# Kernel optimization log

Hardware: AMD Instinct MI355X
Metric: run time of the kernel (lower is better)

The kernel has to match this reference:

```python
import jax, jax.numpy as jnp
import numpy as np

B, L, D, H, E, K = 4, 2048, 1024, 2048, 8, 2


def _mlp(x, w1, b1, w2, b2):
    # Mlp: Linear -> GELU(tanh) -> Linear (dropout disabled / eval mode)
    h = jax.nn.gelu(x @ w1 + b1, approximate=True)
    return h @ w2 + b2


def setup_inputs() -> dict:
    key = jax.random.key(0)
    ks = jax.random.split(key, 16)
    s = 0.02
    inp = {
        "x": jax.random.normal(ks[0], (B, L, D), dtype=jnp.float32),
        "task_ids": jax.random.randint(ks[1], (B,), 0, 9),
        # gate: Linear(D,H) -> GELU -> Linear(H,E)  (zero-init in source; randomized here for a meaningful routing test)
        "gw1": jax.random.normal(ks[2], (D, H), dtype=jnp.float32) * s,
        "gb1": jnp.zeros((H,), dtype=jnp.float32),
        "gw2": jax.random.normal(ks[3], (H, E), dtype=jnp.float32) * s,
        "gb2": jnp.zeros((E,), dtype=jnp.float32),
        # routed experts, stacked [E, ...]
        "We1": jax.random.normal(ks[4], (E, D, H), dtype=jnp.float32) * s,
        "be1": jnp.zeros((E, H), dtype=jnp.float32),
        "We2": jax.random.normal(ks[5], (E, H, D), dtype=jnp.float32) * s,
        "be2": jnp.zeros((E, D), dtype=jnp.float32),
        # shared expert
        "Ws1": jax.random.normal(ks[6], (D, H), dtype=jnp.float32) * s,
        "bs1": jnp.zeros((H,), dtype=jnp.float32),
        "Ws2": jax.random.normal(ks[7], (H, D), dtype=jnp.float32) * s,
        "bs2": jnp.zeros((D,), dtype=jnp.float32),
    }
    return inp


def reference(x, task_ids, gw1, gb1, gw2, gb2, We1, be1, We2, be2, Ws1, bs1, Ws2, bs2):
    bsz, length, d = x.shape
    T = bsz * length
    xf = x.reshape(T, d)

    # ---- top-k gating (single gate: moe_multiple_gate=False) ----
    logits = jax.nn.gelu(xf @ gw1 + gb1, approximate=False) @ gw2 + gb2  # [T, E]
    scores = jax.nn.softmax(logits, axis=-1)
    topk_w, topk_idx = jax.lax.top_k(scores, K)  # [T, K]
    # dense gate matrix: scatter top-k weights back (matches compute_gating's gates)
    rows = jnp.arange(T)[:, None]
    gates = jnp.zeros_like(scores).at[rows, topk_idx].set(topk_w)  # [T, E]

    # ---- shared expert (always applied) ----
    out = _mlp(xf, Ws1, bs1, Ws2, bs2)

    # ---- routed experts: dense-equivalent of sort/dispatch/scatter-combine ----
    # y += sum_e gates[:, e] * expert_e(x); loop over small fixed E to bound memory
    for e in range(E):
        out = out + gates[:, e:e + 1] * _mlp(xf, We1[e], be1[e], We2[e], be2[e])

    return out.reshape(bsz, length, d)
```

## Files before the change

kernel.cpp:

```cpp
#include <hip/hip_runtime.h>
#include <hip/hip_bf16.h>


using bf16 = __hip_bfloat16;
typedef __attribute__((ext_vector_type(8))) short short8;
typedef __attribute__((ext_vector_type(4))) float float4v;

#define T_TOK 8192
#define DDIM  1024
#define HDIM  2048
#define NEXP  8

__device__ __forceinline__ float bf2f(short s) {
  unsigned u = ((unsigned)(unsigned short)s) << 16;
  return __builtin_bit_cast(float, u);
}
__device__ __forceinline__ unsigned short f2bf(float f) {
  unsigned u = __builtin_bit_cast(unsigned, f);
  unsigned r = (u + 0x7fffu + ((u >> 16) & 1u)) >> 16;
  return (unsigned short)r;
}
__device__ __forceinline__ float gelu_erf_f(float x) {
  return 0.5f * x * (1.0f + erff(x * 0.70710678118654752f));
}
__device__ __forceinline__ float gelu_tanh_f(float x) {
  float t = tanhf(0.7978845608028654f * (x + 0.044715f * x * x * x));
  return 0.5f * x * (1.0f + t);
}
__device__ __forceinline__ void gld_lds16(const bf16* g, bf16* l) {
  __builtin_amdgcn_global_load_lds(
      (const __attribute__((address_space(1))) void*)g,
      (__attribute__((address_space(3))) void*)l, 16, 0, 0);
}

__global__ __launch_bounds__(256) void cast_split_x(
    const float* __restrict__ x, bf16* __restrict__ xh, bf16* __restrict__ xl)
{
  long i = ((long)blockIdx.x * 256 + threadIdx.x) * 4;
  float4v v = *(const float4v*)(x + i);
  short4 h, l;
  short* hp = (short*)&h; short* lp = (short*)&l;
  #pragma unroll
  for (int j = 0; j < 4; ++j) {
    unsigned short hb = f2bf(v[j]);
    hp[j] = (short)hb;
    lp[j] = (short)f2bf(v[j] - bf2f((short)hb));
  }
  *(short4*)((short*)xh + i) = h;
  *(short4*)((short*)xl + i) = l;
}

template<bool SPLIT>
__global__ __launch_bounds__(256) void transpose_cast(
    const float* __restrict__ in, bf16* __restrict__ out,
    bf16* __restrict__ outl, int R, int C)
{
  __shared__ float tile[32][33];
  long b = blockIdx.z;
  const float* ip = in + b * (long)R * C;
  short* op = (short*)out + b * (long)R * C;
  short* opl = SPLIT ? (short*)outl + b * (long)R * C : nullptr;
  int c0 = blockIdx.x * 32, r0 = blockIdx.y * 32;
  int tx = threadIdx.x & 31, ty = threadIdx.x >> 5;
  #pragma unroll
  for (int i = ty; i < 32; i += 8)
    tile[i][tx] = ip[(long)(r0 + i) * C + c0 + tx];
  __syncthreads();
  #pragma unroll
  for (int i = ty; i < 32; i += 8) {
    float v = tile[tx][i];
    unsigned short hb = f2bf(v);
    op[(long)(c0 + i) * R + r0 + tx] = (short)hb;
    if (SPLIT)
      opl[(long)(c0 + i) * R + r0 + tx] = (short)f2bf(v - bf2f((short)hb));
  }
}

template<int ACT, typename OutT, int GATHER, bool WEIGHTED, bool SPLIT>
__global__ __launch_bounds__(256) void gemm_bt(
    const bf16* __restrict__ A, const bf16* __restrict__ Bt,
    const bf16* __restrict__ Al, const bf16* __restrict__ Btl,
    const float* __restrict__ bias, OutT* __restrict__ Cmat,
    int M, int N, int Kd, int ldA,
    long strideB, long strideBias,
    const int* __restrict__ perm, const int* __restrict__ counts,
    const float* __restrict__ wslot)
{
  __shared__ __align__(16) bf16 lA[128 * 32];
  __shared__ __align__(16) bf16 lB[128 * 32];
  __shared__ int permT[128];

  const int tid = threadIdx.x;
  const int tile_n = blockIdx.x, tile_m = blockIdx.y, z = blockIdx.z;

  int Meff = M;
  if (GATHER) {
    const int* perm_z = perm + (long)z * T_TOK;
    Meff = counts[z];
    if (tile_m * 128 >= Meff) return;
    if (tid < 128) {
      int i = tile_m * 128 + tid;
      permT[tid] = perm_z[i < Meff ? i : (Meff - 1)];
    }
    __syncthreads();
  }
  const float* biasz = bias + (long)z * strideBias;

  const int i0 = tid >> 2;
  const int kc = (tid & 3) * 8;
  long rowA0, rowA1;
  if (GATHER) {
    int p0 = permT[i0], p1 = permT[i0 + 64];
    rowA0 = (GATHER == 1) ? (p0 >> 1) : p0;
    rowA1 = (GATHER == 1) ? (p1 >> 1) : p1;
  } else {
    rowA0 = (long)tile_m * 128 + i0;
    rowA1 = rowA0 + 64;
  }
  bf16* lA0 = &lA[tid * 8];
  bf16* lA1 = &lA[(tid + 256) * 8];
  bf16* lB0 = &lB[tid * 8];
  bf16* lB1 = &lB[(tid + 256) * 8];

  const int lane = tid & 63;
  const int wave = tid >> 6;
  const int wm = (wave & 1) * 64;
  const int wn = (wave >> 1) * 64;
  const int fr = lane & 15;
  const int fk = (lane >> 4) * 8;

  float4v acc[4][4];
  #pragma unroll
  for (int i = 0; i < 4; ++i)
    #pragma unroll
    for (int j = 0; j < 4; ++j) acc[i][j] = {0.f, 0.f, 0.f, 0.f};

  #pragma unroll 1
  for (int ps = 0; ps < (SPLIT ? 3 : 1); ++ps) {
    const bf16* Ap = (SPLIT && ps == 2) ? Al : A;
    const bf16* Bp = (SPLIT && ps == 1) ? Btl : Bt;
    const bf16* aBase0 = Ap + rowA0 * ldA + kc;
    const bf16* aBase1 = Ap + rowA1 * ldA + kc;
    const bf16* bBase0 = Bp + (long)z * strideB
                       + ((long)tile_n * 128 + i0) * Kd + kc;
    const bf16* bBase1 = bBase0 + (long)64 * Kd;

    for (int k0 = 0; k0 < Kd; k0 += 32) {
      gld_lds16(aBase0 + k0, lA0);
      gld_lds16(aBase1 + k0, lA1);
      gld_lds16(bBase0 + k0, lB0);
      gld_lds16(bBase1 + k0, lB1);
      __syncthreads();

      short8 af[4], bfr[4];
      #pragma unroll
      for (int mi = 0; mi < 4; ++mi)
        af[mi] = *(const short8*)&lA[(wm + mi * 16 + fr) * 32 + fk];
      #pragma unroll
      for (int ni = 0; ni < 4; ++ni)
        bfr[ni] = *(const short8*)&lB[(wn + ni * 16 + fr) * 32 + fk];
      #pragma unroll
      for (int mi = 0; mi < 4; ++mi)
        #pragma unroll
        for (int ni = 0; ni < 4; ++ni)
          acc[mi][ni] = __builtin_amdgcn_mfma_f32_16x16x32_bf16(
              af[mi], bfr[ni], acc[mi][ni], 0, 0, 0);
      __syncthreads();
    }
  }

  const int rq = (lane >> 4) * 4;
  #pragma unroll
  for (int mi = 0; mi < 4; ++mi) {
    #pragma unroll
    for (int r = 0; r < 4; ++r) {
      int irow = wm + mi * 16 + rq + r;
      int gi = tile_m * 128 + irow;
      long crow;
      bool valid = true;
      float w = 1.f;
      if (GATHER) {
        valid = gi < Meff;
        int p = permT[irow];
        crow = p;
        if (WEIGHTED) w = valid ? wslot[p] : 0.f;
      } else {
        crow = gi;
      }
      if (valid) {
        #pragma unroll
        for (int ni = 0; ni < 4; ++ni) {
          int gcol = tile_n * 128 + wn + ni * 16 + fr;
          float v = acc[mi][ni][r] + biasz[gcol];
          if (ACT == 1) v = gelu_erf_f(v);
          else if (ACT == 2) v = gelu_tanh_f(v);
          if (WEIGHTED) v *= w;
          long cidx = crow * (long)N + gcol;
          if (sizeof(OutT) == 4) ((float*)Cmat)[cidx] = v;
          else ((unsigned short*)Cmat)[cidx] = f2bf(v);
        }
      }
    }
  }
}

__global__ __launch_bounds__(256) void logits_kernel(
    const float* __restrict__ G1, const float* __restrict__ gw2,
    const float* __restrict__ gb2, int* __restrict__ tidx,
    float* __restrict__ wslot)
{
  int wv = threadIdx.x >> 6, lane = threadIdx.x & 63;
  int t = blockIdx.x * 4 + wv;
  const float* grow = G1 + (long)t * HDIM;
  float acc[NEXP];
  #pragma unroll
  for (int e = 0; e < NEXP; ++e) acc[e] = 0.f;
  for (int j = 0; j < HDIM / 64; ++j) {
    int h = j * 64 + lane;
    float g = grow[h];
    float4v w0 = *(const float4v*)&gw2[h * NEXP];
    float4v w1 = *(const float4v*)&gw2[h * NEXP + 4];
    #pragma unroll
    for (int e = 0; e < 4; ++e) {
      acc[e]     += g * w0[e];
      acc[e + 4] += g * w1[e];
    }
  }
  #pragma unroll
  for (int off = 32; off >= 1; off >>= 1)
    #pragma unroll
    for (int e = 0; e < NEXP; ++e) acc[e] += __shfl_xor(acc[e], off);

  if (lane == 0) {
    float lg[NEXP];
    #pragma unroll
    for (int e = 0; e < NEXP; ++e) lg[e] = acc[e] + gb2[e];
    int i1 = 0;
    for (int e = 1; e < NEXP; ++e) if (lg[e] > lg[i1]) i1 = e;
    int i2 = (i1 == 0) ? 1 : 0;
    for (int e = 0; e < NEXP; ++e) {
      if (e == i1) continue;
      if (lg[e] > lg[i2]) i2 = e;
    }
    float m = lg[i1], s = 0.f;
    #pragma unroll
    for (int e = 0; e < NEXP; ++e) s += expf(lg[e] - m);
    float inv = 1.f / s;
    tidx[2 * t]     = i1;
    tidx[2 * t + 1] = i2;
    wslot[2 * t]     = expf(lg[i1] - m) * inv;
    wslot[2 * t + 1] = expf(lg[i2] - m) * inv;
  }
}

__global__ __launch_bounds__(256) void dispatch_kernel(
    const int* __restrict__ tidx, int* __restrict__ counts,
    int* __restrict__ perm)
{
  int t = blockIdx.x * 256 + threadIdx.x;
  int lane = threadIdx.x & 63;
  #pragma unroll
  for (int k = 0; k < 2; ++k) {
    int e = tidx[2 * t + k];
    #pragma unroll
    for (int ex = 0; ex < NEXP; ++ex) {
      unsigned long long m = __ballot(e == ex);
      if (m) {
        int leader = __ffsll((unsigned long long)m) - 1;
        int base = 0;
        if (lane == leader) base = atomicAdd(&counts[ex], __popcll(m));
        base = __shfl(base, leader);
        if (e == ex) {
          int pos = base + __popcll(m & ((1ULL << lane) - 1ULL));
          perm[ex * T_TOK + pos] = 2 * t + k;
        }
      }
    }
  }
}

__global__ __launch_bounds__(256) void combine_kernel(
    const bf16* __restrict__ Rout, float* __restrict__ out)
{
  long idx = (long)blockIdx.x * 256 + threadIdx.x;
  long t = idx >> 7;
  long dc = idx & 127;
  const short* rs = (const short*)Rout;
  short8 a = *(const short8*)&rs[(2 * t) * DDIM + dc * 8];
  short8 b = *(const short8*)&rs[(2 * t + 1) * DDIM + dc * 8];
  float* op = out + idx * 8;
  float4v o0 = *(const float4v*)op;
  float4v o1 = *(const float4v*)(op + 4);
  #pragma unroll
  for (int j = 0; j < 4; ++j) o0[j] += bf2f(a[j]) + bf2f(b[j]);
  #pragma unroll
  for (int j = 0; j < 4; ++j) o1[j] += bf2f(a[j + 4]) + bf2f(b[j + 4]);
  *(float4v*)op = o0;
  *(float4v*)(op + 4) = o1;
}

extern "C" void kernel_launch(void* const* d_in, const int* in_sizes, int n_in,
                              void* d_out, int out_size, void* d_ws, size_t ws_size,
                              hipStream_t stream)
{
  const float* x   = (const float*)d_in[0];
  const float* gw1 = (const float*)d_in[2];
  const float* gb1 = (const float*)d_in[3];
  const float* gw2 = (const float*)d_in[4];
  const float* gb2 = (const float*)d_in[5];
  const float* We1 = (const float*)d_in[6];
  const float* be1 = (const float*)d_in[7];
  const float* We2 = (const float*)d_in[8];
  const float* be2 = (const float*)d_in[9];
  const float* Ws1 = (const float*)d_in[10];
  const float* bs1 = (const float*)d_in[11];
  const float* Ws2 = (const float*)d_in[12];
  const float* bs2 = (const float*)d_in[13];
  float* out = (float*)d_out;

  char* ws = (char*)d_ws;
  bf16*  xb     = (bf16*)(ws + 0);
  bf16*  We1t   = (bf16*)(ws + 16777216);
  bf16*  Rout   = (bf16*)(ws + 16777216);
  bf16*  We2t   = (bf16*)(ws + 50331648);
  bf16*  Ws1t   = (bf16*)(ws + 83886080);
  bf16*  Ws2t   = (bf16*)(ws + 88080384);
  int*   counts = (int*)(ws + 92274688);
  float* wslot  = (float*)(ws + 92275712);
  int*   perm   = (int*)(ws + 92341248);
  bf16*  xl     = (bf16*)(ws + 92603392);
  bf16*  gw1h   = (bf16*)(ws + 109380608);
  bf16*  gw1l   = (bf16*)(ws + 113574912);
  int*   tidx   = (int*)(ws + 113574912);
  float* G1     = (float*)(ws + 117769216);
  bf16*  S1     = (bf16*)(ws + 117769216);
  bf16*  Hrt    = (bf16*)(ws + 117769216);

  hipMemsetAsync(counts, 0, NEXP * sizeof(int), stream);

  dim3 blk(256);
  cast_split_x<<<dim3((T_TOK * DDIM) / 1024), blk, 0, stream>>>(x, xb, xl);
  transpose_cast<true ><<<dim3(HDIM/32, DDIM/32, 1), blk, 0, stream>>>(gw1, gw1h, gw1l, DDIM, HDIM);
  transpose_cast<false><<<dim3(HDIM/32, DDIM/32, 1), blk, 0, stream>>>(Ws1, Ws1t, nullptr, DDIM, HDIM);
  transpose_cast<false><<<dim3(DDIM/32, HDIM/32, 1), blk, 0, stream>>>(Ws2, Ws2t, nullptr, HDIM, DDIM);
  transpose_cast<false><<<dim3(HDIM/32, DDIM/32, NEXP), blk, 0, stream>>>(We1, We1t, nullptr, DDIM, HDIM);
  transpose_cast<false><<<dim3(DDIM/32, HDIM/32, NEXP), blk, 0, stream>>>(We2, We2t, nullptr, HDIM, DDIM);

  gemm_bt<1, float, 0, false, true><<<dim3(HDIM/128, T_TOK/128, 1), blk, 0, stream>>>(
      xb, gw1h, xl, gw1l, gb1, G1, T_TOK, HDIM, DDIM, DDIM, 0, 0,
      nullptr, nullptr, nullptr);
  logits_kernel<<<dim3(T_TOK / 4), blk, 0, stream>>>(G1, gw2, gb2, tidx, wslot);
  dispatch_kernel<<<dim3(T_TOK / 256), blk, 0, stream>>>(tidx, counts, perm);
  gemm_bt<2, bf16, 0, false, false><<<dim3(HDIM/128, T_TOK/128, 1), blk, 0, stream>>>(
      xb, Ws1t, nullptr, nullptr, bs1, S1, T_TOK, HDIM, DDIM, DDIM, 0, 0,
      nullptr, nullptr, nullptr);
  gemm_bt<0, float, 0, false, false><<<dim3(DDIM/128, T_TOK/128, 1), blk, 0, stream>>>(
      S1, Ws2t, nullptr, nullptr, bs2, out, T_TOK, DDIM, HDIM, HDIM, 0, 0,
      nullptr, nullptr, nullptr);
  gemm_bt<2, bf16, 1, false, false><<<dim3(HDIM/128, T_TOK/128, NEXP), blk, 0, stream>>>(
      xb, We1t, nullptr, nullptr, be1, Hrt, T_TOK, HDIM, DDIM, DDIM,
      (long)HDIM * DDIM, HDIM, perm, counts, nullptr);
  gemm_bt<0, bf16, 2, true, false><<<dim3(DDIM/128, T_TOK/128, NEXP), blk, 0, stream>>>(
      Hrt, We2t, nullptr, nullptr, be2, Rout, T_TOK, DDIM, HDIM, HDIM,
      (long)DDIM * HDIM, DDIM, perm, counts, wslot);
  combine_kernel<<<dim3((T_TOK * DDIM) / 2048), blk, 0, stream>>>(Rout, out);
}
```

Measured before the change: 901.6 us.

## Fuse routed-expert combine into shared-expert GEMM epilogue and XOR-swizzle LDS tiles

The routed-expert GEMMs now run before the shared-expert MLP. The final shared GEMM epilogue reads the two weighted bf16 routed outputs per token and adds them before writing fp32 output, so the separate combine kernel and its extra read-modify-write pass over the output go away. The LDS tile layout also gets an XOR swizzle of the 16-byte k-chunk by row index, on both the global-to-LDS writes and the MFMA fragment reads, to cut bank conflicts on the 64-byte row stride. The trade-off is that the fused epilogue does scalar, less-coalesced bf16 loads of Rout inside the GEMM, and the new launch order depends on Rout staying intact while later kernels write their buffers.

```diff
diff --git a/kernel.cpp b/kernel.cpp
--- a/kernel.cpp
+++ b/kernel.cpp
@@ -76,7 +76,7 @@
   }
 }
 
-template<int ACT, typename OutT, int GATHER, bool WEIGHTED, bool SPLIT>
+template<int ACT, typename OutT, int GATHER, bool WEIGHTED, bool SPLIT, bool COMBINE>
 __global__ __launch_bounds__(256) void gemm_bt(
     const bf16* __restrict__ A, const bf16* __restrict__ Bt,
     const bf16* __restrict__ Al, const bf16* __restrict__ Btl,
@@ -84,7 +84,7 @@
     int M, int N, int Kd, int ldA,
     long strideB, long strideBias,
     const int* __restrict__ perm, const int* __restrict__ counts,
-    const float* __restrict__ wslot)
+    const float* __restrict__ wslot, const bf16* __restrict__ RoutC)
 {
   __shared__ __align__(16) bf16 lA[128 * 32];
   __shared__ __align__(16) bf16 lB[128 * 32];
@@ -107,7 +107,7 @@
   const float* biasz = bias + (long)z * strideBias;
 
   const int i0 = tid >> 2;
-  const int kc = (tid & 3) * 8;
+  const int kc = (((tid & 3) ^ ((tid >> 2) & 3))) * 8;
   long rowA0, rowA1;
   if (GATHER) {
     int p0 = permT[i0], p1 = permT[i0 + 64];
@@ -127,7 +127,7 @@
   const int wm = (wave & 1) * 64;
   const int wn = (wave >> 1) * 64;
   const int fr = lane & 15;
-  const int fk = (lane >> 4) * 8;
+  const int sw = (((lane >> 4) ^ (lane & 3))) * 8;
 
   float4v acc[4][4];
   #pragma unroll
@@ -155,10 +155,10 @@
       short8 af[4], bfr[4];
       #pragma unroll
       for (int mi = 0; mi < 4; ++mi)
-        af[mi] = *(const short8*)&lA[(wm + mi * 16 + fr) * 32 + fk];
+        af[mi] = *(const short8*)&lA[(wm + mi * 16 + fr) * 32 + sw];
       #pragma unroll
       for (int ni = 0; ni < 4; ++ni)
-        bfr[ni] = *(const short8*)&lB[(wn + ni * 16 + fr) * 32 + fk];
+        bfr[ni] = *(const short8*)&lB[(wn + ni * 16 + fr) * 32 + sw];
       #pragma unroll
       for (int mi = 0; mi < 4; ++mi)
         #pragma unroll
@@ -169,7 +169,7 @@
     }
   }
 
-  const int rq = (lane >> 4) * 4;
+  const int rq = ((lane >> 4)) * 4;
   #pragma unroll
   for (int mi = 0; mi < 4; ++mi) {
     #pragma unroll
@@ -195,6 +195,11 @@
           if (ACT == 1) v = gelu_erf_f(v);
           else if (ACT == 2) v = gelu_tanh_f(v);
           if (WEIGHTED) v *= w;
+          if (COMBINE) {
+            const short* rs = (const short*)RoutC;
+            v += bf2f(rs[(2 * crow) * DDIM + gcol])
+               + bf2f(rs[(2 * crow + 1) * DDIM + gcol]);
+          }
           long cidx = crow * (long)N + gcol;
           if (sizeof(OutT) == 4) ((float*)Cmat)[cidx] = v;
           else ((unsigned short*)Cmat)[cidx] = f2bf(v);
@@ -277,26 +282,6 @@
       }
     }
   }
-}
-
-__global__ __launch_bounds__(256) void combine_kernel(
-    const bf16* __restrict__ Rout, float* __restrict__ out)
-{
-  long idx = (long)blockIdx.x * 256 + threadIdx.x;
-  long t = idx >> 7;
-  long dc = idx & 127;
-  const short* rs = (const short*)Rout;
-  short8 a = *(const short8*)&rs[(2 * t) * DDIM + dc * 8];
-  short8 b = *(const short8*)&rs[(2 * t + 1) * DDIM + dc * 8];
-  float* op = out + idx * 8;
-  float4v o0 = *(const float4v*)op;
-  float4v o1 = *(const float4v*)(op + 4);
-  #pragma unroll
-  for (int j = 0; j < 4; ++j) o0[j] += bf2f(a[j]) + bf2f(b[j]);
-  #pragma unroll
-  for (int j = 0; j < 4; ++j) o1[j] += bf2f(a[j + 4]) + bf2f(b[j + 4]);
-  *(float4v*)op = o0;
-  *(float4v*)(op + 4) = o1;
 }
 
 extern "C" void kernel_launch(void* const* d_in, const int* in_sizes, int n_in,
@@ -333,8 +318,8 @@
   bf16*  gw1l   = (bf16*)(ws + 113574912);
   int*   tidx   = (int*)(ws + 113574912);
   float* G1     = (float*)(ws + 117769216);
+  bf16*  Hrt    = (bf16*)(ws + 117769216);
   bf16*  S1     = (bf16*)(ws + 117769216);
-  bf16*  Hrt    = (bf16*)(ws + 117769216);
 
   hipMemsetAsync(counts, 0, NEXP * sizeof(int), stream);
 
@@ -346,22 +331,21 @@
   transpose_cast<false><<<dim3(HDIM/32, DDIM/32, NEXP), blk, 0, stream>>>(We1, We1t, nullptr, DDIM, HDIM);
   transpose_cast<false><<<dim3(DDIM/32, HDIM/32, NEXP), blk, 0, stream>>>(We2, We2t, nullptr, HDIM, DDIM);
 
-  gemm_bt<1, float, 0, false, true><<<dim3(HDIM/128, T_TOK/128, 1), blk, 0, stream>>>(
+  gemm_bt<1, float, 0, false, true, false><<<dim3(HDIM/128, T_TOK/128, 1), blk, 0, stream>>>(
       xb, gw1h, xl, gw1l, gb1, G1, T_TOK, HDIM, DDIM, DDIM, 0, 0,
-      nullptr, nullptr, nullptr);
+      nullptr, nullptr, nullptr, nullptr);
   logits_kernel<<<dim3(T_TOK / 4), blk, 0, stream>>>(G1, gw2, gb2, tidx, wslot);
   dispatch_kernel<<<dim3(T_TOK / 256), blk, 0, stream>>>(tidx, counts, perm);
-  gemm_bt<2, bf16, 0, false, false><<<dim3(HDIM/128, T_TOK/128, 1), blk, 0, stream>>>(
+  gemm_bt<2, bf16, 1, false, false, false><<<dim3(HDIM/128, T_TOK/128, NEXP), blk, 0, stream>>>(
+      xb, We1t, nullptr, nullptr, be1, Hrt, T_TOK, HDIM, DDIM, DDIM,
+      (long)HDIM * DDIM, HDIM, perm, counts, nullptr, nullptr);
+  gemm_bt<0, bf16, 2, true, false, false><<<dim3(DDIM/128, T_TOK/128, NEXP), blk, 0, stream>>>(
+      Hrt, We2t, nullptr, nullptr, be2, Rout, T_TOK, DDIM, HDIM, HDIM,
+      (long)DDIM * HDIM, DDIM, perm, counts, wslot, nullptr);
+  gemm_bt<2, bf16, 0, false, false, false><<<dim3(HDIM/128, T_TOK/128, 1), blk, 0, stream>>>(
       xb, Ws1t, nullptr, nullptr, bs1, S1, T_TOK, HDIM, DDIM, DDIM, 0, 0,
-      nullptr, nullptr, nullptr);
-  gemm_bt<0, float, 0, false, false><<<dim3(DDIM/128, T_TOK/128, 1), blk, 0, stream>>>(
+      nullptr, nullptr, nullptr, nullptr);
+  gemm_bt<0, float, 0, false, false, true><<<dim3(DDIM/128, T_TOK/128, 1), blk, 0, stream>>>(
       S1, Ws2t, nullptr, nullptr, bs2, out, T_TOK, DDIM, HDIM, HDIM, 0, 0,
-      nullptr, nullptr, nullptr);
-  gemm_bt<2, bf16, 1, false, false><<<dim3(HDIM/128, T_TOK/128, NEXP), blk, 0, stream>>>(
-      xb, We1t, nullptr, nullptr, be1, Hrt, T_TOK, HDIM, DDIM, DDIM,
-      (long)HDIM * DDIM, HDIM, perm, counts, nullptr);
-  gemm_bt<0, bf16, 2, true, false><<<dim3(DDIM/128, T_TOK/128, NEXP), blk, 0, stream>>>(
-      Hrt, We2t, nullptr, nullptr, be2, Rout, T_TOK, DDIM, HDIM, HDIM,
-      (long)DDIM * HDIM, DDIM, perm, counts, wslot);
-  combine_kernel<<<dim3((T_TOK * DDIM) / 2048), blk, 0, stream>>>(Rout, out);
-}
+      nullptr, nullptr, nullptr, Rout);
+}
```

Result: no change. 884.3 us (-1.9%).
